# Performance work log

Hardware: AMD Instinct MI355X
Metric: run time of the kernel (lower is better)

## Reference

```python
import jax, jax.numpy as jnp
import numpy as np

D_MODEL = 1024

def setup_inputs() -> dict:
    key = jax.random.key(0)
    k1, k2 = jax.random.split(key, 2)
    x = jax.random.normal(k1, (4, 2048, D_MODEL), dtype=jnp.float32)
    W_attn = jax.random.normal(k2, (3 * D_MODEL, D_MODEL), dtype=jnp.float32) * (1.0 / np.sqrt(D_MODEL))
    b_attn = jnp.zeros((3 * D_MODEL,), dtype=jnp.float32)
    return {"x": x, "W_attn": W_attn, "b_attn": b_attn}

def reference(x, W_attn, b_attn):
    B, T, C = x.shape
    # fused QKV projection; torch split order is (k, q, v)
    kqv = x @ W_attn.T + b_attn            # [B, T, 3C]
    k, q, v = jnp.split(kqv, 3, axis=-1)   # each [B, T, C]
    # NOTE: original computes k @ q^T (quirk), scaled by sqrt(d_model)
    scores = jnp.einsum('btc,bsc->bts', k, q) / jnp.sqrt(jnp.asarray(C, x.dtype))
    causal = jnp.tril(jnp.ones((T, T), dtype=bool))
    scores = jnp.where(causal[None, :, :], scores, -jnp.inf)
    attn = jax.nn.softmax(scores, axis=-1)
    return jnp.einsum('bts,bsc->btc', attn, v)
```

## Files before the change

### kernel.cpp

```cpp
#include <hip/hip_runtime.h>

typedef __bf16 bf16x8 __attribute__((ext_vector_type(8)));
typedef float f32x4 __attribute__((ext_vector_type(4)));
typedef float fl4 __attribute__((ext_vector_type(4)));
typedef unsigned short us4 __attribute__((ext_vector_type(4)));
typedef unsigned short us8 __attribute__((ext_vector_type(8)));

__device__ __forceinline__ unsigned short f2bf(float f) {
  unsigned u = __builtin_bit_cast(unsigned, f);
  u += 0x7fffu + ((u >> 16) & 1u);
  return (unsigned short)(u >> 16);
}
__device__ __forceinline__ float bf2f(unsigned short h) {
  unsigned u = ((unsigned)h) << 16;
  return __builtin_bit_cast(float, u);
}

__device__ __forceinline__ void async16(const void* g, void* l) {
  __builtin_amdgcn_global_load_lds(
      (const __attribute__((address_space(1))) unsigned int*)g,
      (__attribute__((address_space(3))) unsigned int*)l, 16, 0, 0);
}

#define BARM() asm volatile("s_barrier" ::: "memory")
#define VMCNT4() asm volatile("s_waitcnt vmcnt(4)" ::: "memory")
#define LGKM0() asm volatile("s_waitcnt lgkmcnt(0)" ::: "memory")

__global__ __launch_bounds__(256) void cvt_bf16(const float* __restrict__ s,
                                                unsigned short* __restrict__ d, int n4) {
  int i = blockIdx.x * 256 + threadIdx.x;
  if (i >= n4) return;
  fl4 f = ((const fl4*)s)[i];
  us4 o;
  o[0] = f2bf(f[0]); o[1] = f2bf(f[1]); o[2] = f2bf(f[2]); o[3] = f2bf(f[3]);
  ((us4*)d)[i] = o;
}

__global__ __launch_bounds__(256) void transpose_v(const unsigned short* __restrict__ kqv,
                                                   unsigned short* __restrict__ vT) {
  int b = blockIdx.z;
  int t0 = blockIdx.x * 64;
  int c0 = blockIdx.y * 64;
  __shared__ unsigned short tile[64][68];
  int tid = threadIdx.x;
#pragma unroll
  for (int i = 0; i < 4; ++i) {
    int idx = i * 256 + tid;
    int r = idx >> 4;
    int c4 = (idx & 15) * 4;
    const unsigned short* src = kqv + ((size_t)(b * 2048 + t0 + r)) * 3072 + 2048 + c0 + c4;
    us4 v = *(const us4*)src;
    *(us4*)&tile[r][c4] = v;
  }
  __syncthreads();
#pragma unroll
  for (int i = 0; i < 4; ++i) {
    int idx = i * 256 + tid;
    int rc = idx >> 4;
    int t4 = (idx & 15) * 4;
    us4 v;
    v[0] = tile[t4 + 0][rc]; v[1] = tile[t4 + 1][rc];
    v[2] = tile[t4 + 2][rc]; v[3] = tile[t4 + 3][rc];
    unsigned short* dst = vT + ((size_t)(b * 1024 + c0 + rc)) * 2048 + t0 + t4;
    *(us4*)dst = v;
  }
}

template <int EPI>
__global__ __launch_bounds__(512, 2) void gemm8p(
    const unsigned short* __restrict__ A, int lda, long long sA,
    const unsigned short* __restrict__ B, int ldb, long long sB,
    void* __restrict__ Cv, int ldc, long long sC,
    const float* __restrict__ bias, float scale, int K, int NBX) {
  int bx, by;
  const int bz = blockIdx.z;
  if (EPI == 0) {
    int flat = blockIdx.x;
    int q = (int)gridDim.x >> 3;
    int swz = (flat & 7) * q + (flat >> 3);
    bx = swz % NBX; by = swz / NBX;
  } else {
    bx = blockIdx.x; by = blockIdx.y;
    if (EPI == 1 && bx > by) return;
  }
  A += (size_t)bz * sA;
  B += (size_t)bz * sB;
  const int rowBase = by * 256;
  const int colBase = bx * 256;
  const int nk = (EPI == 2) ? (rowBase + 256) / 64 : K / 64;

  __shared__ __align__(16) unsigned char lds[131072];
  const int tid = threadIdx.x;
  const int lane = tid & 63;
  const int wid = tid >> 6;
  const int wr = wid >> 2;
  const int wc = wid & 3;
  const int l15 = lane & 15, l4 = lane >> 4, l7 = lane & 7;

  f32x4 acc[8][4] = {};
  bf16x8 af0[4], af1[4], bf0[4], bf1[4];

  const unsigned short* Ab = A + (size_t)rowBase * lda;
  const unsigned short* Bb = B + (size_t)colBase * ldb;
  unsigned loff[2][2];
  unsigned lldso[2];
#pragma unroll
  for (int i = 0; i < 2; ++i) {
    int off = (i * 512 + tid) * 16;
    int r = off >> 7;
    int sb = ((off >> 4) & 7) ^ (r & 7);
    lldso[i] = (unsigned)off;
#pragma unroll
    for (int h = 0; h < 2; ++h)
      loff[h][i] = (unsigned)((h * 128 + r) * lda + sb * 8);
  }

  auto STAGE = [&](int bufc, int isB, int half, const unsigned short* Gb, int koff) {
#pragma unroll
    for (int i = 0; i < 2; ++i)
      async16(Gb + (size_t)(loff[half][i] + (unsigned)koff),
              lds + bufc * 65536 + isB * 32768 + half * 16384 + lldso[i]);
  };
  auto RDA = [&](int bufc, int m, int kk) -> bf16x8 {
    int row = m * 16 + l15;
    int blk = (kk * 4 + l4) ^ l7;
    return *(const bf16x8*)(lds + bufc * 65536 + wr * 16384 + row * 128 + blk * 16);
  };
  auto RDB = [&](int bufc, int n, int kk) -> bf16x8 {
    int row = (wc & 1) * 64 + n * 16 + l15;
    int blk = (kk * 4 + l4) ^ l7;
    return *(const bf16x8*)(lds + bufc * 65536 + 32768 + (wc >> 1) * 16384 +
                            row * 128 + blk * 16);
  };

#define RDAF(dst, BUF, MB, KK)                                                 \
  _Pragma("unroll") for (int mi = 0; mi < 4; ++mi) dst[mi] = RDA((BUF), (MB) + mi, (KK))
#define RDBF2(dst, BUF, N0, KK)                                                \
  do { dst[N0] = RDB((BUF), (N0), (KK)); dst[(N0) + 1] = RDB((BUF), (N0) + 1, (KK)); } while (0)
#define RDBF4(dst, BUF, KK)                                                    \
  _Pragma("unroll") for (int n = 0; n < 4; ++n) dst[n] = RDB((BUF), n, (KK))

#define PH(MB, AFU, BFU, STG, GATE, RDS)                                       \
  do {                                                                         \
    STG;                                                                       \
    BARM();                                                                    \
    GATE;                                                                      \
    RDS;                                                                       \
    __builtin_amdgcn_s_setprio(1);                                             \
    _Pragma("unroll") for (int mi = 0; mi < 4; ++mi)                           \
    _Pragma("unroll") for (int n = 0; n < 4; ++n)                              \
        acc[(MB) + mi][n] = __builtin_amdgcn_mfma_f32_16x16x32_bf16(           \
            AFU[mi], BFU[n], acc[(MB) + mi][n], 0, 0, 0);                      \
    __builtin_amdgcn_s_setprio(0);                                             \
    LGKM0();                                                                   \
    BARM();                                                                    \
  } while (0)

  STAGE(0, 0, 0, Ab, 0);
  STAGE(0, 0, 1, Ab, 0);
  STAGE(0, 1, 0, Bb, 0);
  STAGE(0, 1, 1, Bb, 0);
  {
    int k1 = ((1 < nk - 1) ? 1 : (nk - 1)) * 64;
    STAGE(1, 1, 0, Bb, k1);
    STAGE(1, 1, 1, Bb, k1);
  }
  VMCNT4();
  BARM();
  RDAF(af0, 0, 0, 0);
  RDBF4(bf0, 0, 0);
  const int nt2 = nk >> 1;
  for (int it = 0; it < nt2; ++it) {
    int t = it * 2;
    int tA1 = t + 1 < nk - 1 ? t + 1 : nk - 1;
    int t2 = t + 2 < nk - 1 ? t + 2 : nk - 1;
    int t3 = t + 3 < nk - 1 ? t + 3 : nk - 1;
    int kA1 = tA1 * 64, k2 = t2 * 64, k3 = t3 * 64;
    PH(0, af0, bf0, STAGE(1, 0, 0, Ab, kA1), (void)0,
       { RDAF(af1, 0, 4, 0); RDBF2(bf1, 0, 0, 1); });
    PH(4, af1, bf0, STAGE(1, 0, 1, Ab, kA1), (void)0,
       { RDAF(af0, 0, 0, 1); RDBF2(bf1, 0, 2, 1); });
    PH(0, af0, bf1, STAGE(0, 1, 0, Bb, k2), (void)0,
       { RDAF(af1, 0, 4, 1); });
    PH(4, af1, bf1, STAGE(0, 1, 1, Bb, k2), VMCNT4(),
       { RDAF(af0, 1, 0, 0); RDBF4(bf0, 1, 0); });
    PH(0, af0, bf0, STAGE(0, 0, 0, Ab, k2), (void)0,
       { RDAF(af1, 1, 4, 0); RDBF2(bf1, 1, 0, 1); });
    PH(4, af1, bf0, STAGE(0, 0, 1, Ab, k2), (void)0,
       { RDAF(af0, 1, 0, 1); RDBF2(bf1, 1, 2, 1); });
    PH(0, af0, bf1, STAGE(1, 1, 0, Bb, k3), (void)0,
       { RDAF(af1, 1, 4, 1); });
    PH(4, af1, bf1, STAGE(1, 1, 1, Bb, k3), VMCNT4(),
       { RDAF(af0, 0, 0, 0); RDBF4(bf0, 0, 0); });
  }
#undef PH
#undef RDAF
#undef RDBF2
#undef RDBF4

  const int cr = l4 * 4;
  if constexpr (EPI == 0) {
    unsigned short* C = (unsigned short*)Cv;
#pragma unroll
    for (int n = 0; n < 4; ++n) {
      int col = colBase + wc * 64 + n * 16 + l15;
      float bv = bias[col];
#pragma unroll
      for (int m = 0; m < 8; ++m) {
        int row = rowBase + wr * 128 + m * 16 + cr;
#pragma unroll
        for (int i = 0; i < 4; ++i)
          C[(size_t)(row + i) * ldc + col] = f2bf(acc[m][n][i] + bv);
      }
    }
  } else if constexpr (EPI == 1) {
    unsigned short* C = (unsigned short*)Cv + (size_t)bz * sC;
#pragma unroll
    for (int n = 0; n < 4; ++n) {
      int col = colBase + wc * 64 + n * 16 + l15;
#pragma unroll
      for (int m = 0; m < 8; ++m) {
        int row = rowBase + wr * 128 + m * 16 + cr;
#pragma unroll
        for (int i = 0; i < 4; ++i)
          C[(size_t)(row + i) * ldc + col] = f2bf(acc[m][n][i] * scale);
      }
    }
  } else {
    float* C = (float*)Cv + (size_t)bz * sC;
#pragma unroll
    for (int n = 0; n < 4; ++n) {
      int col = colBase + wc * 64 + n * 16 + l15;
#pragma unroll
      for (int m = 0; m < 8; ++m) {
        int row = rowBase + wr * 128 + m * 16 + cr;
#pragma unroll
        for (int i = 0; i < 4; ++i)
          C[(size_t)(row + i) * ldc + col] = acc[m][n][i];
      }
    }
  }
}

__global__ __launch_bounds__(256) void softmax_causal(unsigned short* __restrict__ S) {
  const int T = 2048;
  int t = blockIdx.x, b = blockIdx.y;
  unsigned short* row = S + ((size_t)b * T + t) * T;
  const int nv = t + 1;
  int tid = threadIdx.x;
  int lane = tid & 63, wid = tid >> 6;
  int s0 = tid * 8;
  us8 raw = *(const us8*)(row + s0);
  float v[8];
  float m = -3.0e38f;
#pragma unroll
  for (int j = 0; j < 8; ++j) {
    v[j] = bf2f(raw[j]);
    if (s0 + j < nv) m = fmaxf(m, v[j]);
  }
#pragma unroll
  for (int o = 32; o > 0; o >>= 1) m = fmaxf(m, __shfl_xor(m, o, 64));
  __shared__ float red[4];
  if (lane == 0) red[wid] = m;
  __syncthreads();
  m = fmaxf(fmaxf(red[0], red[1]), fmaxf(red[2], red[3]));
  __syncthreads();
  float sum = 0.f;
#pragma unroll
  for (int j = 0; j < 8; ++j) {
    float e = (s0 + j < nv) ? exp2f(v[j] - m) : 0.f;
    v[j] = e;
    sum += e;
  }
#pragma unroll
  for (int o = 32; o > 0; o >>= 1) sum += __shfl_xor(sum, o, 64);
  if (lane == 0) red[wid] = sum;
  __syncthreads();
  sum = red[0] + red[1] + red[2] + red[3];
  float inv = 1.0f / sum;
  us8 outv;
#pragma unroll
  for (int j = 0; j < 8; ++j) outv[j] = f2bf(v[j] * inv);
  *(us8*)(row + s0) = outv;
}

extern "C" void kernel_launch(void* const* d_in, const int* in_sizes, int n_in,
                              void* d_out, int out_size, void* d_ws, size_t ws_size,
                              hipStream_t stream) {
  const float* x = (const float*)d_in[0];
  const float* W = (const float*)d_in[1];
  const float* bias = (const float*)d_in[2];
  float* out = (float*)d_out;

  char* ws = (char*)d_ws;
  if (ws_size < 106954752u) return;
  unsigned short* xbf = (unsigned short*)(ws);
  unsigned short* vT = xbf;
  unsigned short* wbf = (unsigned short*)(ws + 16777216);
  unsigned short* kqv = (unsigned short*)(ws + 23068672);
  unsigned short* S = (unsigned short*)(ws + 73400320);

  const float kSoftmaxScale = 1.4426950408889634f / 32.0f;

  cvt_bf16<<<8192, 256, 0, stream>>>(x, xbf, 2097152);
  cvt_bf16<<<3072, 256, 0, stream>>>(W, wbf, 786432);

  gemm8p<0><<<dim3(384, 1, 1), 512, 0, stream>>>(
      xbf, 1024, 0LL, wbf, 1024, 0LL, kqv, 3072, 0LL, bias, 1.0f, 1024, 12);

  transpose_v<<<dim3(32, 16, 4), 256, 0, stream>>>(kqv, vT);

  gemm8p<1><<<dim3(8, 8, 4), 512, 0, stream>>>(
      kqv, 3072, 2048LL * 3072, kqv + 1024, 3072, 2048LL * 3072,
      S, 2048, 2048LL * 2048, nullptr, kSoftmaxScale, 1024, 0);

  softmax_causal<<<dim3(2048, 4), 256, 0, stream>>>(S);

  gemm8p<2><<<dim3(4, 8, 4), 512, 0, stream>>>(
      S, 2048, 2048LL * 2048, vT, 2048, 1024LL * 2048,
      out, 1024, 2048LL * 1024, nullptr, 1.0f, 2048, 0);
}
```

Before: 189.7 us.

## Restructure GEMM LDS read schedule, merge conversion kernels, trim softmax masked I/O

The GEMM main loop now issues each phase's LDS fragment reads up front as larger 4x2 by 2x2 register quadrants. It waits on lgkmcnt before the MFMA block, which sits behind a scheduling barrier, so the 2x2 MFMA quadrants reuse fragments across k-steps. The two fp32-to-bf16 conversion launches become one combined launch. The causal softmax skips loading fully masked chunks and writes only up to the next 256-aligned bound, which is the only region the PV GEMM reads. These changes raise register pressure and reorder waits in the GEMM, so latency hiding may change in either direction.

```diff
diff --git a/kernel.cpp b/kernel.cpp
--- a/kernel.cpp
+++ b/kernel.cpp
@@ -25,11 +25,23 @@
 #define BARM() asm volatile("s_barrier" ::: "memory")
 #define VMCNT4() asm volatile("s_waitcnt vmcnt(4)" ::: "memory")
 #define LGKM0() asm volatile("s_waitcnt lgkmcnt(0)" ::: "memory")
-
-__global__ __launch_bounds__(256) void cvt_bf16(const float* __restrict__ s,
-                                                unsigned short* __restrict__ d, int n4) {
+#define LGKM8() asm volatile("s_waitcnt lgkmcnt(8)" ::: "memory")
+#define SCHEDB() __builtin_amdgcn_sched_barrier(0)
+
+__global__ __launch_bounds__(256) void cvt_bf16_2(const float* __restrict__ sA,
+                                                  unsigned short* __restrict__ dA, int nA,
+                                                  const float* __restrict__ sB,
+                                                  unsigned short* __restrict__ dB, int nB) {
   int i = blockIdx.x * 256 + threadIdx.x;
-  if (i >= n4) return;
+  const float* s;
+  unsigned short* d;
+  if (i < nA) {
+    s = sA; d = dA;
+  } else {
+    i -= nA;
+    if (i >= nB) return;
+    s = sB; d = dB;
+  }
   fl4 f = ((const fl4*)s)[i];
   us4 o;
   o[0] = f2bf(f[0]); o[1] = f2bf(f[1]); o[2] = f2bf(f[2]); o[3] = f2bf(f[3]);
@@ -98,7 +110,7 @@
   const int l15 = lane & 15, l4 = lane >> 4, l7 = lane & 7;
 
   f32x4 acc[8][4] = {};
-  bf16x8 af0[4], af1[4], bf0[4], bf1[4];
+  bf16x8 af0[4][2], af1[4][2], bf0[2][2], bf1[2][2];
 
   const unsigned short* Ab = A + (size_t)rowBase * lda;
   const unsigned short* Bb = B + (size_t)colBase * ldb;
@@ -133,26 +145,34 @@
                             row * 128 + blk * 16);
   };
 
-#define RDAF(dst, BUF, MB, KK)                                                 \
-  _Pragma("unroll") for (int mi = 0; mi < 4; ++mi) dst[mi] = RDA((BUF), (MB) + mi, (KK))
-#define RDBF2(dst, BUF, N0, KK)                                                \
-  do { dst[N0] = RDB((BUF), (N0), (KK)); dst[(N0) + 1] = RDB((BUF), (N0) + 1, (KK)); } while (0)
-#define RDBF4(dst, BUF, KK)                                                    \
-  _Pragma("unroll") for (int n = 0; n < 4; ++n) dst[n] = RDB((BUF), n, (KK))
-
-#define PH(MB, AFU, BFU, STG, GATE, RDS)                                       \
+#define RDA8(dst, BUF, Q)                                                      \
+  _Pragma("unroll") for (int mi = 0; mi < 4; ++mi)                             \
+  _Pragma("unroll") for (int kk = 0; kk < 2; ++kk)                             \
+      dst[mi][kk] = RDA((BUF), (Q) * 4 + mi, kk)
+#define RDB4(dst, BUF, NB)                                                     \
+  _Pragma("unroll") for (int nj = 0; nj < 2; ++nj)                             \
+  _Pragma("unroll") for (int kk = 0; kk < 2; ++kk)                             \
+      dst[nj][kk] = RDB((BUF), (NB) + nj, kk)
+
+#define MFMAQ(MB, NB, AF, BF)                                                  \
+  _Pragma("unroll") for (int kk = 0; kk < 2; ++kk)                             \
+  _Pragma("unroll") for (int mi = 0; mi < 4; ++mi)                             \
+  _Pragma("unroll") for (int nj = 0; nj < 2; ++nj)                             \
+      acc[(MB) + mi][(NB) + nj] = __builtin_amdgcn_mfma_f32_16x16x32_bf16(     \
+          AF[mi][kk], BF[nj][kk], acc[(MB) + mi][(NB) + nj], 0, 0, 0)
+
+#define PH(RDS, STG, HINT, GATE, MB, NB, AF, BF)                               \
   do {                                                                         \
+    RDS;                                                                       \
     STG;                                                                       \
+    HINT;                                                                      \
     BARM();                                                                    \
+    LGKM0();                                                                   \
+    SCHEDB();                                                                  \
+    __builtin_amdgcn_s_setprio(1);                                             \
+    MFMAQ(MB, NB, AF, BF);                                                     \
+    __builtin_amdgcn_s_setprio(0);                                             \
     GATE;                                                                      \
-    RDS;                                                                       \
-    __builtin_amdgcn_s_setprio(1);                                             \
-    _Pragma("unroll") for (int mi = 0; mi < 4; ++mi)                           \
-    _Pragma("unroll") for (int n = 0; n < 4; ++n)                              \
-        acc[(MB) + mi][n] = __builtin_amdgcn_mfma_f32_16x16x32_bf16(           \
-            AFU[mi], BFU[n], acc[(MB) + mi][n], 0, 0, 0);                      \
-    __builtin_amdgcn_s_setprio(0);                                             \
-    LGKM0();                                                                   \
     BARM();                                                                    \
   } while (0)
 
@@ -160,43 +180,38 @@
   STAGE(0, 0, 1, Ab, 0);
   STAGE(0, 1, 0, Bb, 0);
   STAGE(0, 1, 1, Bb, 0);
-  {
-    int k1 = ((1 < nk - 1) ? 1 : (nk - 1)) * 64;
-    STAGE(1, 1, 0, Bb, k1);
-    STAGE(1, 1, 1, Bb, k1);
-  }
+  STAGE(1, 1, 0, Bb, 64);
+  STAGE(1, 1, 1, Bb, 64);
   VMCNT4();
   BARM();
-  RDAF(af0, 0, 0, 0);
-  RDBF4(bf0, 0, 0);
+
   const int nt2 = nk >> 1;
   for (int it = 0; it < nt2; ++it) {
     int t = it * 2;
-    int tA1 = t + 1 < nk - 1 ? t + 1 : nk - 1;
-    int t2 = t + 2 < nk - 1 ? t + 2 : nk - 1;
-    int t3 = t + 3 < nk - 1 ? t + 3 : nk - 1;
-    int kA1 = tA1 * 64, k2 = t2 * 64, k3 = t3 * 64;
-    PH(0, af0, bf0, STAGE(1, 0, 0, Ab, kA1), (void)0,
-       { RDAF(af1, 0, 4, 0); RDBF2(bf1, 0, 0, 1); });
-    PH(4, af1, bf0, STAGE(1, 0, 1, Ab, kA1), (void)0,
-       { RDAF(af0, 0, 0, 1); RDBF2(bf1, 0, 2, 1); });
-    PH(0, af0, bf1, STAGE(0, 1, 0, Bb, k2), (void)0,
-       { RDAF(af1, 0, 4, 1); });
-    PH(4, af1, bf1, STAGE(0, 1, 1, Bb, k2), VMCNT4(),
-       { RDAF(af0, 1, 0, 0); RDBF4(bf0, 1, 0); });
-    PH(0, af0, bf0, STAGE(0, 0, 0, Ab, k2), (void)0,
-       { RDAF(af1, 1, 4, 0); RDBF2(bf1, 1, 0, 1); });
-    PH(4, af1, bf0, STAGE(0, 0, 1, Ab, k2), (void)0,
-       { RDAF(af0, 1, 0, 1); RDBF2(bf1, 1, 2, 1); });
-    PH(0, af0, bf1, STAGE(1, 1, 0, Bb, k3), (void)0,
-       { RDAF(af1, 1, 4, 1); });
-    PH(4, af1, bf1, STAGE(1, 1, 1, Bb, k3), VMCNT4(),
-       { RDAF(af0, 0, 0, 0); RDBF4(bf0, 0, 0); });
+    int kA1 = (t + 1) * 64;
+    int k2 = (t + 2 < nk - 1 ? t + 2 : nk - 1) * 64;
+    int k3 = (t + 3 < nk - 1 ? t + 3 : nk - 1) * 64;
+    PH({ RDA8(af0, 0, 0); RDB4(bf0, 0, 0); }, STAGE(1, 0, 0, Ab, kA1), LGKM8(),
+       (void)0, 0, 0, af0, bf0);
+    PH({ RDB4(bf1, 0, 2); }, STAGE(1, 0, 1, Ab, kA1), (void)0,
+       (void)0, 0, 2, af0, bf1);
+    PH({ RDA8(af1, 0, 1); }, STAGE(0, 1, 0, Bb, k2), (void)0,
+       (void)0, 4, 2, af1, bf1);
+    PH({}, STAGE(0, 1, 1, Bb, k2), (void)0,
+       VMCNT4(), 4, 0, af1, bf0);
+    PH({ RDA8(af0, 1, 0); RDB4(bf0, 1, 0); }, STAGE(0, 0, 0, Ab, k2), LGKM8(),
+       (void)0, 0, 0, af0, bf0);
+    PH({ RDB4(bf1, 1, 2); }, STAGE(0, 0, 1, Ab, k2), (void)0,
+       (void)0, 0, 2, af0, bf1);
+    PH({ RDA8(af1, 1, 1); }, STAGE(1, 1, 0, Bb, k3), (void)0,
+       (void)0, 4, 2, af1, bf1);
+    PH({}, STAGE(1, 1, 1, Bb, k3), (void)0,
+       VMCNT4(), 4, 0, af1, bf0);
   }
 #undef PH
-#undef RDAF
-#undef RDBF2
-#undef RDBF4
+#undef MFMAQ
+#undef RDA8
+#undef RDB4
 
   const int cr = l4 * 4;
   if constexpr (EPI == 0) {
@@ -247,10 +262,12 @@
   int t = blockIdx.x, b = blockIdx.y;
   unsigned short* row = S + ((size_t)b * T + t) * T;
   const int nv = t + 1;
+  const int bound = ((t >> 8) + 1) << 8;
   int tid = threadIdx.x;
   int lane = tid & 63, wid = tid >> 6;
   int s0 = tid * 8;
-  us8 raw = *(const us8*)(row + s0);
+  us8 raw = {};
+  if (s0 < nv) raw = *(const us8*)(row + s0);
   float v[8];
   float m = -3.0e38f;
 #pragma unroll
@@ -278,10 +295,12 @@
   __syncthreads();
   sum = red[0] + red[1] + red[2] + red[3];
   float inv = 1.0f / sum;
-  us8 outv;
-#pragma unroll
-  for (int j = 0; j < 8; ++j) outv[j] = f2bf(v[j] * inv);
-  *(us8*)(row + s0) = outv;
+  if (s0 < bound) {
+    us8 outv;
+#pragma unroll
+    for (int j = 0; j < 8; ++j) outv[j] = f2bf(v[j] * inv);
+    *(us8*)(row + s0) = outv;
+  }
 }
 
 extern "C" void kernel_launch(void* const* d_in, const int* in_sizes, int n_in,
@@ -302,8 +321,7 @@
 
   const float kSoftmaxScale = 1.4426950408889634f / 32.0f;
 
-  cvt_bf16<<<8192, 256, 0, stream>>>(x, xbf, 2097152);
-  cvt_bf16<<<3072, 256, 0, stream>>>(W, wbf, 786432);
+  cvt_bf16_2<<<11264, 256, 0, stream>>>(x, xbf, 2097152, W, wbf, 786432);
 
   gemm8p<0><<<dim3(384, 1, 1), 512, 0, stream>>>(
       xbf, 1024, 0LL, wbf, 1024, 0LL, kqv, 3072, 0LL, bias, 1.0f, 1024, 12);
```

After: 189.6 us. No clear change (-0.1%).
